# Kernel tuning notes

Measured on AMD Instinct MI355X. Metric: run time of the kernel, lower is better.

Reference implementation:

```python
import jax, jax.numpy as jnp
import numpy as np

H, I, B = 256, 128, 512

def setup_inputs() -> dict:
    key = jax.random.key(0)
    ks = jax.random.split(key, 24)
    n = lambda k, shp, s=1.0: jax.random.normal(k, shp, dtype=jnp.float32) * s
    inp = {
        "x": n(ks[0], (B, I)),
        "hx": n(ks[1], (B, H), 0.1),
        "cx": n(ks[2], (B, H, H), 0.1),
        # input->gate weights (hidden, input), xavier-like scale
        "Wii": n(ks[3], (H, I), (2.0 / (H + I)) ** 0.5),
        "Wif": n(ks[4], (H, I), (2.0 / (H + I)) ** 0.5),
        "Wig": n(ks[5], (H, I), (2.0 / (H + I)) ** 0.5),
        "Wio": n(ks[6], (H, I), (2.0 / (H + I)) ** 0.5),
        # hidden->gate weights (hidden, hidden), ~orthogonal scale
        "Whi": n(ks[7], (H, H), H ** -0.5),
        "Whit": n(ks[8], (H, H), H ** -0.5),
        "Whf": n(ks[9], (H, H), H ** -0.5),
        "Whft": n(ks[10], (H, H), H ** -0.5),
        "Whc": n(ks[11], (H, H), H ** -0.5),
        "Whct": n(ks[12], (H, H), H ** -0.5),
        "Who": n(ks[13], (H, H), H ** -0.5),
        "Uinv": n(ks[14], (H, H), H ** -0.5),
        "Vtinv": n(ks[15], (H, H), H ** -0.5),
        # biases: bi/bf/bg are full (H,H) matrices, bo is (H,1)
        "bi": jnp.zeros((H, H), jnp.float32),
        "bf": jnp.zeros((H, H), jnp.float32),
        "bg": jnp.zeros((H, H), jnp.float32),
        "bo": jnp.zeros((H, 1), jnp.float32),
    }
    return inp


def reference(x, hx, cx, Wii, Wif, Wig, Wio, Whi, Whit, Whf, Whft, Whc, Whct, Who, Uinv, Vtinv, bi, bf, bg, bo):
    # W @ diag(v) @ M^T  ==  einsum('hi,bi,gi->bhg', W, v, M)
    def sandwich(Wx, Wh, Wht, b):
        # (Wx*x) @ Wx^T + (Wh*hx) @ Wht^T + b  -> (B,H,H)
        xt = jnp.einsum('hi,bi,gi->bhg', Wx, x, Wx)
        ht = jnp.einsum('hj,bj,gj->bhg', Wh, hx, Wht)
        return xt + ht + b

    i = jax.nn.sigmoid(sandwich(Wii, Whi, Whit, bi))
    f = jax.nn.sigmoid(sandwich(Wif, Whf, Whft, bf))
    g = jnp.tanh(sandwich(Wig, Whc, Whct, bg))
    # o: ordinary vector gate (B,H)
    o = jax.nn.sigmoid(jnp.einsum('hi,bi->bh', Wio, x)
                       + jnp.einsum('hj,bj->bh', Who, hx) + bo[:, 0])
    cx_new = f * cx + i * g                     # (B,H,H)
    # diag(Uinv @ cx_new @ Vtinv) per batch element -> (B,H)
    proj_down = jnp.einsum('ij,bjk,ki->bi', Uinv, cx_new, Vtinv)
    hx_new = o * jax.nn.sigmoid(proj_down)
    return hx_new
```

## Files before the change

### kernel.cpp

```cpp
#include <hip/hip_runtime.h>
#include <hip/hip_bf16.h>

#define Hh 256
#define Ii 128
#define KF 384
#define KB 64
#define BK 64
#define LDSB 72

typedef __attribute__((ext_vector_type(8))) short bf16x8;
typedef __attribute__((ext_vector_type(4))) float f32x4;
typedef unsigned short u16;
typedef unsigned int u32;

__device__ inline float bf2f(u16 u) { return __uint_as_float(((u32)u) << 16); }
__device__ inline u16 f2bf(float f) {
  u32 u = __float_as_uint(f);
  u += 0x7FFFu + ((u >> 16) & 1u);
  return (u16)(u >> 16);
}
__device__ inline u32 pack_bf16x2(float a, float b) {
  __hip_bfloat162 h = __float22bfloat162_rn(make_float2(a, b));
  u32 r; __builtin_memcpy(&r, &h, 4); return r;
}
__device__ inline u32 scale2(u32 packed, float va, float vb) {
  float lo = __uint_as_float(packed << 16) * va;
  float hi = __uint_as_float(packed & 0xFFFF0000u) * vb;
  return pack_bf16x2(lo, hi);
}
__device__ inline float sigm(float x) { return 1.0f / (1.0f + __expf(-x)); }
__device__ inline float tanh_f(float x) { return 1.0f - 2.0f / (1.0f + __expf(2.0f * x)); }

union U32x4 { bf16x8 f; u32 d[4]; uint4 v; };

__global__ __launch_bounds__(256) void k_prep(
    const float* __restrict__ Wii, const float* __restrict__ Wif, const float* __restrict__ Wig,
    const float* __restrict__ Whi, const float* __restrict__ Whit,
    const float* __restrict__ Whf, const float* __restrict__ Whft,
    const float* __restrict__ Whc, const float* __restrict__ Whct,
    const float* __restrict__ Vtinv, const float* __restrict__ Uinv,
    const float* __restrict__ bi, const float* __restrict__ bfm, const float* __restrict__ bg,
    u16* __restrict__ RW, u16* __restrict__ CW, u16* __restrict__ Vtt,
    u16* __restrict__ biasP, float* __restrict__ UinvP, float* __restrict__ proj) {
  const int tid = threadIdx.x, bx = blockIdx.x, y = blockIdx.y;
  if (y < 3) {
    const float* WX  = (y == 0) ? Wii : (y == 1 ? Wif : Wig);
    const float* WHr = (y == 0) ? Whi : (y == 1 ? Whf : Whc);
    const float* WHt = (y == 0) ? Whit : (y == 1 ? Whft : Whct);
    u16* rw = RW + y * Hh * KF;
    u16* cw = CW + y * Hh * KF;
#pragma unroll
    for (int it = 0; it < 4; ++it) {
      int idx = it * 24576 + bx * 256 + tid;
      int h = idx / KF, t = idx - h * KF;
      float a, c;
      if (t < Ii) { a = WX[h * Ii + t]; c = a; }
      else        { a = WHr[h * Hh + t - Ii]; c = WHt[h * Hh + t - Ii]; }
      rw[idx] = f2bf(a);
      cw[idx] = f2bf(c);
    }
  } else if (y == 3) {
    if (bx < 64) {
      __shared__ u16 tbuf[32][33];
      const int c = tid & 31, r8 = tid >> 5;
      const int tr = bx >> 3, tc = bx & 7;
#pragma unroll
      for (int rr = r8; rr < 32; rr += 8)
        tbuf[rr][c] = f2bf(Vtinv[(tc * 32 + rr) * Hh + tr * 32 + c]);
      __syncthreads();
#pragma unroll
      for (int rr = r8; rr < 32; rr += 8)
        Vtt[(tr * 32 + rr) * Hh + tc * 32 + c] = tbuf[c][rr];
    } else if (bx < 96) {
      const int base = (bx - 64) * 256 + tid;
      const float4 z = {0.f, 0.f, 0.f, 0.f};
#pragma unroll
      for (int it = 0; it < 4; ++it)
        *(float4*)(proj + (size_t)(it * 8192 + base) * 4) = z;
    }
  } else if (y == 4) {
    const int base = (bx * 256 + tid) * 8;
#pragma unroll
    for (int e8 = 0; e8 < 8; ++e8) {
      int f = base + e8;
      int ph = f >> 16;
      int r1 = f & 65535;
      int jb = r1 >> 14;
      int r2 = r1 & 16383;
      int kb = r2 >> 12;
      int r3 = r2 & 4095;
      int t  = r3 >> 4;
      int e  = r3 & 15;
      int w = t >> 6, quad = (t >> 4) & 3, r15 = t & 15;
      int tk = e >> 2, rr = e & 3;
      int j   = jb * 64 + w * 16 + quad * 4 + rr;
      int col = kb * 64 + tk * 16 + r15;
      const float* src = (ph == 0) ? bg : (ph == 1 ? bi : bfm);
      biasP[f] = f2bf(src[j * Hh + col]);
    }
  } else {
    if (bx < 32) {
      const int base = (bx * 256 + tid) * 8;
#pragma unroll
      for (int e8 = 0; e8 < 8; ++e8) {
        int f = base + e8;
        int jb = f >> 14;
        int r2 = f & 16383;
        int t  = r2 >> 6;
        int e  = r2 & 63;
        int ti = e >> 4, tj = (e >> 2) & 3, rr = e & 3;
        int w = t >> 6, quad = (t >> 4) & 3, r15 = t & 15;
        int i = w * 64 + ti * 16 + quad * 4 + rr;
        int j = jb * 64 + tj * 16 + r15;
        UinvP[f] = Uinv[i * Hh + j];
      }
    }
  }
}

__global__ __launch_bounds__(256) void k_main(
    const float* __restrict__ x, const float* __restrict__ hx, const float* __restrict__ cx,
    const u16* __restrict__ RW, const u16* __restrict__ CW,
    const u16* __restrict__ Vtt, const u16* __restrict__ biasP,
    const float* __restrict__ UinvP, float* __restrict__ proj) {
  __shared__ u16 sB[2 * KB * LDSB];
  __shared__ u16 sP[KB * LDSB];
  __shared__ float sV[KF];

  const int tid  = threadIdx.x;
  const int b    = blockIdx.x >> 4;
  const int jb   = (blockIdx.x >> 2) & 3;
  const int kb   = blockIdx.x & 3;
  const int k0   = kb * KB;
  const int lane = tid & 63;
  const int w    = tid >> 6;
  const int r15  = lane & 15;
  const int quad = lane >> 4;
  const int jbase = jb * 64 + w * 16;
  const int brow = tid >> 2, bcg = tid & 3;

  if (tid < Ii) sV[tid] = x[b * Ii + tid];
  sV[Ii + tid] = hx[b * Hh + tid];

  const u16* rwp[3] = {RW + 2 * Hh * KF, RW, RW + 1 * Hh * KF};
  const u16* cwp[3] = {CW + 2 * Hh * KF, CW, CW + 1 * Hh * KF};
  const float* cx_b = cx + (size_t)b * Hh * Hh;

  __syncthreads();

  U32x4 n0, n1;
  {
    const u16* src = cwp[0] + (size_t)(k0 + brow) * KF + bcg * 16;
    n0.v = *(const uint4*)src;
    n1.v = *(const uint4*)(src + 8);
  }
  bf16x8 fa[2];
  fa[0] = *(const bf16x8*)(rwp[0] + (size_t)(jbase + r15) * KF + quad * 8);
  fa[1] = *(const bf16x8*)(rwp[0] + (size_t)(jbase + r15) * KF + 32 + quad * 8);
  {
    U32x4 o0, o1;
    const float4 v0 = *(const float4*)(&sV[bcg * 16]);
    const float4 v1 = *(const float4*)(&sV[bcg * 16 + 4]);
    const float4 v2 = *(const float4*)(&sV[bcg * 16 + 8]);
    const float4 v3 = *(const float4*)(&sV[bcg * 16 + 12]);
    o0.d[0] = scale2(n0.d[0], v0.x, v0.y); o0.d[1] = scale2(n0.d[1], v0.z, v0.w);
    o0.d[2] = scale2(n0.d[2], v1.x, v1.y); o0.d[3] = scale2(n0.d[3], v1.z, v1.w);
    o1.d[0] = scale2(n1.d[0], v2.x, v2.y); o1.d[1] = scale2(n1.d[1], v2.z, v2.w);
    o1.d[2] = scale2(n1.d[2], v3.x, v3.y); o1.d[3] = scale2(n1.d[3], v3.z, v3.w);
    u16* dst = sB + brow * LDSB + bcg * 16;
    *(uint4*)dst = o0.v;
    *(uint4*)(dst + 8) = o1.v;
  }
  __syncthreads();

  float p[4][4];

#pragma unroll
  for (int ph = 0; ph < 3; ++ph) {
    f32x4 acc[4];
#pragma unroll
    for (int tk = 0; tk < 4; ++tk)
#pragma unroll
      for (int r = 0; r < 4; ++r) acc[tk][r] = 0.0f;

#pragma unroll
    for (int kc = 0; kc < 6; ++kc) {
      const int sc = ph * 6 + kc;
      const int cur = sc & 1;
      const int nph = (kc < 5) ? ph : (ph < 2 ? ph + 1 : 0);
      const int nt0 = (kc < 5) ? (kc + 1) * BK : 0;
      U32x4 m0, m1;
      bf16x8 fan[2];
      if (sc < 17) {
        const u16* src = cwp[nph] + (size_t)(k0 + brow) * KF + nt0 + bcg * 16;
        m0.v = *(const uint4*)src;
        m1.v = *(const uint4*)(src + 8);
        fan[0] = *(const bf16x8*)(rwp[nph] + (size_t)(jbase + r15) * KF + nt0 + quad * 8);
        fan[1] = *(const bf16x8*)(rwp[nph] + (size_t)(jbase + r15) * KF + nt0 + 32 + quad * 8);
      }
#pragma unroll
      for (int ks = 0; ks < 2; ++ks) {
        bf16x8 fb[4];
#pragma unroll
        for (int tk = 0; tk < 4; ++tk)
          fb[tk] = *(const bf16x8*)(&sB[cur * (KB * LDSB) + (tk * 16 + r15) * LDSB + ks * 32 + quad * 8]);
#pragma unroll
        for (int tk = 0; tk < 4; ++tk)
          acc[tk] = __builtin_amdgcn_mfma_f32_16x16x32_bf16(fa[ks], fb[tk], acc[tk], 0, 0, 0);
      }
      if (sc < 17) {
        U32x4 o0, o1;
        const float4 v0 = *(const float4*)(&sV[nt0 + bcg * 16]);
        const float4 v1 = *(const float4*)(&sV[nt0 + bcg * 16 + 4]);
        const float4 v2 = *(const float4*)(&sV[nt0 + bcg * 16 + 8]);
        const float4 v3 = *(const float4*)(&sV[nt0 + bcg * 16 + 12]);
        o0.d[0] = scale2(m0.d[0], v0.x, v0.y); o0.d[1] = scale2(m0.d[1], v0.z, v0.w);
        o0.d[2] = scale2(m0.d[2], v1.x, v1.y); o0.d[3] = scale2(m0.d[3], v1.z, v1.w);
        o1.d[0] = scale2(m1.d[0], v2.x, v2.y); o1.d[1] = scale2(m1.d[1], v2.z, v2.w);
        o1.d[2] = scale2(m1.d[2], v3.x, v3.y); o1.d[3] = scale2(m1.d[3], v3.z, v3.w);
        u16* dst = sB + (cur ^ 1) * (KB * LDSB) + brow * LDSB + bcg * 16;
        *(uint4*)dst = o0.v;
        *(uint4*)(dst + 8) = o1.v;
        fa[0] = fan[0];
        fa[1] = fan[1];
      }
      if (kc == 5) {
        const u16* bp = biasP + ((size_t)((ph * 4 + jb) * 4 + kb) * 256 + tid) * 16;
        const uint4 b0 = *(const uint4*)bp;
        const uint4 b1 = *(const uint4*)(bp + 8);
        const u32 bw[8] = {b0.x, b0.y, b0.z, b0.w, b1.x, b1.y, b1.z, b1.w};
        if (ph == 2) {
          float cxv[16];
#pragma unroll
          for (int tk = 0; tk < 4; ++tk)
#pragma unroll
            for (int r = 0; r < 4; ++r)
              cxv[tk * 4 + r] = cx_b[(size_t)(jbase + quad * 4 + r) * Hh + k0 + tk * 16 + r15];
#pragma unroll
          for (int tk = 0; tk < 4; ++tk)
#pragma unroll
            for (int r = 0; r < 4; ++r) {
              const int e = tk * 4 + r;
              const float bias = (e & 1) ? __uint_as_float(bw[e >> 1] & 0xFFFF0000u)
                                         : __uint_as_float(bw[e >> 1] << 16);
              const float z = acc[tk][r] + bias;
              const float c = sigm(z) * cxv[e] + p[tk][r];
              sP[(w * 16 + quad * 4 + r) * LDSB + tk * 16 + r15] = f2bf(c);
            }
        } else {
#pragma unroll
          for (int tk = 0; tk < 4; ++tk)
#pragma unroll
            for (int r = 0; r < 4; ++r) {
              const int e = tk * 4 + r;
              const float bias = (e & 1) ? __uint_as_float(bw[e >> 1] & 0xFFFF0000u)
                                         : __uint_as_float(bw[e >> 1] << 16);
              const float z = acc[tk][r] + bias;
              if (ph == 0) p[tk][r] = tanh_f(z);
              else         p[tk][r] *= sigm(z);
            }
        }
      }
      __syncthreads();
    }
  }

  bf16x8 fbp[2][4];
#pragma unroll
  for (int ks = 0; ks < 2; ++ks)
#pragma unroll
    for (int tj = 0; tj < 4; ++tj)
      fbp[ks][tj] = *(const bf16x8*)(&sP[(tj * 16 + r15) * LDSB + ks * 32 + quad * 8]);

  float racc[4][4];
#pragma unroll
  for (int ti = 0; ti < 4; ++ti)
#pragma unroll
    for (int r = 0; r < 4; ++r) racc[ti][r] = 0.0f;

  const float* up = UinvP + ((size_t)jb * 256 + tid) * 64;
#pragma unroll
  for (int ti = 0; ti < 4; ++ti) {
    const bf16x8 va0 = *(const bf16x8*)(Vtt + (size_t)(w * 64 + ti * 16 + r15) * Hh + k0 + quad * 8);
    const bf16x8 va1 = *(const bf16x8*)(Vtt + (size_t)(w * 64 + ti * 16 + r15) * Hh + k0 + 32 + quad * 8);
    f32x4 pacc[4];
#pragma unroll
    for (int tj = 0; tj < 4; ++tj)
#pragma unroll
      for (int r = 0; r < 4; ++r) pacc[tj][r] = 0.0f;
#pragma unroll
    for (int tj = 0; tj < 4; ++tj)
      pacc[tj] = __builtin_amdgcn_mfma_f32_16x16x32_bf16(va0, fbp[0][tj], pacc[tj], 0, 0, 0);
#pragma unroll
    for (int tj = 0; tj < 4; ++tj)
      pacc[tj] = __builtin_amdgcn_mfma_f32_16x16x32_bf16(va1, fbp[1][tj], pacc[tj], 0, 0, 0);
    const float4 u0 = *(const float4*)(up + ti * 16);
    const float4 u1 = *(const float4*)(up + ti * 16 + 4);
    const float4 u2 = *(const float4*)(up + ti * 16 + 8);
    const float4 u3 = *(const float4*)(up + ti * 16 + 12);
    const float uu[16] = {u0.x, u0.y, u0.z, u0.w, u1.x, u1.y, u1.z, u1.w,
                          u2.x, u2.y, u2.z, u2.w, u3.x, u3.y, u3.z, u3.w};
#pragma unroll
    for (int tj = 0; tj < 4; ++tj)
#pragma unroll
      for (int r = 0; r < 4; ++r)
        racc[ti][r] += pacc[tj][r] * uu[tj * 4 + r];
  }

#pragma unroll
  for (int ti = 0; ti < 4; ++ti)
#pragma unroll
    for (int r = 0; r < 4; ++r) {
      float v = racc[ti][r];
      v += __shfl_xor(v, 1);
      v += __shfl_xor(v, 2);
      v += __shfl_xor(v, 4);
      v += __shfl_xor(v, 8);
      if (r15 == 0) atomicAdd(&proj[b * Hh + w * 64 + ti * 16 + quad * 4 + r], v);
    }
}

__global__ __launch_bounds__(256) void k_out(
    const float* __restrict__ x, const float* __restrict__ hx,
    const float* __restrict__ Wio, const float* __restrict__ Who,
    const float* __restrict__ bo, const float* __restrict__ proj,
    float* __restrict__ out) {
  __shared__ float sv[KF];
  const int b = blockIdx.x, tid = threadIdx.x;
  const int lane = tid & 63, w = tid >> 6;
  if (tid < Ii) sv[tid] = x[b * Ii + tid];
  sv[Ii + tid] = hx[b * Hh + tid];
  __syncthreads();
  for (int rr = 0; rr < 64; ++rr) {
    const int h = w * 64 + rr;
    float p = Wio[h * Ii + lane]        * sv[lane]
            + Wio[h * Ii + 64 + lane]   * sv[64 + lane]
            + Who[h * Hh + lane]        * sv[128 + lane]
            + Who[h * Hh + 64 + lane]   * sv[192 + lane]
            + Who[h * Hh + 128 + lane]  * sv[256 + lane]
            + Who[h * Hh + 192 + lane]  * sv[320 + lane];
    p += __shfl_xor(p, 32);
    p += __shfl_xor(p, 16);
    p += __shfl_xor(p, 8);
    p += __shfl_xor(p, 4);
    p += __shfl_xor(p, 2);
    p += __shfl_xor(p, 1);
    if (lane == 0)
      out[b * Hh + h] = sigm(p + bo[h]) * sigm(proj[b * Hh + h]);
  }
}

extern "C" void kernel_launch(void* const* d_in, const int* in_sizes, int n_in,
                              void* d_out, int out_size, void* d_ws, size_t ws_size,
                              hipStream_t stream) {
  (void)in_sizes; (void)n_in; (void)out_size; (void)ws_size;
  const float* x    = (const float*)d_in[0];
  const float* hx   = (const float*)d_in[1];
  const float* cx   = (const float*)d_in[2];
  const float* Wii  = (const float*)d_in[3];
  const float* Wif  = (const float*)d_in[4];
  const float* Wig  = (const float*)d_in[5];
  const float* Wio  = (const float*)d_in[6];
  const float* Whi  = (const float*)d_in[7];
  const float* Whit = (const float*)d_in[8];
  const float* Whf  = (const float*)d_in[9];
  const float* Whft = (const float*)d_in[10];
  const float* Whc  = (const float*)d_in[11];
  const float* Whct = (const float*)d_in[12];
  const float* Who  = (const float*)d_in[13];
  const float* Uinv = (const float*)d_in[14];
  const float* Vtinv= (const float*)d_in[15];
  const float* bi   = (const float*)d_in[16];
  const float* bf   = (const float*)d_in[17];
  const float* bg   = (const float*)d_in[18];
  const float* bo   = (const float*)d_in[19];
  float* out = (float*)d_out;

  u16* RW    = (u16*)d_ws;
  u16* CW    = RW + 3 * Hh * KF;
  u16* Vtt   = CW + 3 * Hh * KF;
  u16* biasP = Vtt + Hh * Hh;
  float* UinvP = (float*)(biasP + 3 * Hh * Hh);
  float* proj  = UinvP + Hh * Hh;

  k_prep<<<dim3(96, 6), 256, 0, stream>>>(Wii, Wif, Wig, Whi, Whit, Whf, Whft, Whc, Whct,
                                          Vtinv, Uinv, bi, bf, bg,
                                          RW, CW, Vtt, biasP, UinvP, proj);
  k_main<<<8192, 256, 0, stream>>>(x, hx, cx, RW, CW, Vtt, biasP, UinvP, proj);
  k_out<<<512, 256, 0, stream>>>(x, hx, Wio, Who, bo, proj, out);
}
```

Before: 563.0 us.

## Widen main kernel blocks to cover all 256 rows per batch-column tile

k_main now launches 2048 blocks of 512 threads, each covering the full 256-row j range for one batch and 64-column k slice, instead of 8192 blocks of 256 threads each covering 64 rows. The scaled cx-weight tile in LDS is built once per block and reused across four times as many rows, so the redundant global loads and rescaling are removed, and each wave now computes two 16-row MFMA tiles. Biases are read directly from the fp32 inputs rather than from a pre-permuted bf16 copy, so that prep step is dropped. Partial projection sums are combined in shared memory before a single atomic per output, which cuts atomic traffic. The cost is a larger sP buffer in LDS and more registers per thread, which may reduce occupancy.

```diff
diff --git a/kernel.cpp b/kernel.cpp
--- a/kernel.cpp
+++ b/kernel.cpp
@@ -4,8 +4,6 @@
 #define Hh 256
 #define Ii 128
 #define KF 384
-#define KB 64
-#define BK 64
 #define LDSB 72
 
 typedef __attribute__((ext_vector_type(8))) short bf16x8;
@@ -13,7 +11,6 @@
 typedef unsigned short u16;
 typedef unsigned int u32;
 
-__device__ inline float bf2f(u16 u) { return __uint_as_float(((u32)u) << 16); }
 __device__ inline u16 f2bf(float f) {
   u32 u = __float_as_uint(f);
   u += 0x7FFFu + ((u >> 16) & 1u);
@@ -39,9 +36,8 @@
     const float* __restrict__ Whf, const float* __restrict__ Whft,
     const float* __restrict__ Whc, const float* __restrict__ Whct,
     const float* __restrict__ Vtinv, const float* __restrict__ Uinv,
-    const float* __restrict__ bi, const float* __restrict__ bfm, const float* __restrict__ bg,
     u16* __restrict__ RW, u16* __restrict__ CW, u16* __restrict__ Vtt,
-    u16* __restrict__ biasP, float* __restrict__ UinvP, float* __restrict__ proj) {
+    float* __restrict__ UinvP, float* __restrict__ proj) {
   const int tid = threadIdx.x, bx = blockIdx.x, y = blockIdx.y;
   if (y < 3) {
     const float* WX  = (y == 0) ? Wii : (y == 1 ? Wif : Wig);
@@ -78,233 +74,197 @@
       for (int it = 0; it < 4; ++it)
         *(float4*)(proj + (size_t)(it * 8192 + base) * 4) = z;
     }
-  } else if (y == 4) {
-    const int base = (bx * 256 + tid) * 8;
-#pragma unroll
-    for (int e8 = 0; e8 < 8; ++e8) {
-      int f = base + e8;
-      int ph = f >> 16;
-      int r1 = f & 65535;
-      int jb = r1 >> 14;
-      int r2 = r1 & 16383;
-      int kb = r2 >> 12;
-      int r3 = r2 & 4095;
-      int t  = r3 >> 4;
-      int e  = r3 & 15;
-      int w = t >> 6, quad = (t >> 4) & 3, r15 = t & 15;
-      int tk = e >> 2, rr = e & 3;
-      int j   = jb * 64 + w * 16 + quad * 4 + rr;
-      int col = kb * 64 + tk * 16 + r15;
-      const float* src = (ph == 0) ? bg : (ph == 1 ? bi : bfm);
-      biasP[f] = f2bf(src[j * Hh + col]);
-    }
   } else {
     if (bx < 32) {
       const int base = (bx * 256 + tid) * 8;
 #pragma unroll
       for (int e8 = 0; e8 < 8; ++e8) {
         int f = base + e8;
-        int jb = f >> 14;
-        int r2 = f & 16383;
-        int t  = r2 >> 6;
-        int e  = r2 & 63;
-        int ti = e >> 4, tj = (e >> 2) & 3, rr = e & 3;
-        int w = t >> 6, quad = (t >> 4) & 3, r15 = t & 15;
-        int i = w * 64 + ti * 16 + quad * 4 + rr;
-        int j = jb * 64 + tj * 16 + r15;
+        int t512 = f >> 7;
+        int e = f & 127;
+        int ti = e >> 5;
+        int rem = e & 31;
+        int tjl = rem >> 2;
+        int rr = rem & 3;
+        int wv = t512 >> 6;
+        int ln = t512 & 63;
+        int qd = ln >> 4;
+        int r15v = ln & 15;
+        int i = (wv & 3) * 64 + ti * 16 + qd * 4 + rr;
+        int j = (wv >> 2) * 128 + tjl * 16 + r15v;
         UinvP[f] = Uinv[i * Hh + j];
       }
     }
   }
 }
 
-__global__ __launch_bounds__(256) void k_main(
+__global__ __launch_bounds__(512, 4) void k_main(
     const float* __restrict__ x, const float* __restrict__ hx, const float* __restrict__ cx,
-    const u16* __restrict__ RW, const u16* __restrict__ CW,
-    const u16* __restrict__ Vtt, const u16* __restrict__ biasP,
+    const u16* __restrict__ RW, const u16* __restrict__ CW, const u16* __restrict__ Vtt,
+    const float* __restrict__ bi, const float* __restrict__ bfm, const float* __restrict__ bg,
     const float* __restrict__ UinvP, float* __restrict__ proj) {
-  __shared__ u16 sB[2 * KB * LDSB];
-  __shared__ u16 sP[KB * LDSB];
+  __shared__ u16 sB[2 * 64 * LDSB];
+  __shared__ u16 sP[256 * LDSB];
   __shared__ float sV[KF];
+  __shared__ float sPart[8][64];
 
   const int tid  = threadIdx.x;
-  const int b    = blockIdx.x >> 4;
-  const int jb   = (blockIdx.x >> 2) & 3;
+  const int b    = blockIdx.x >> 2;
   const int kb   = blockIdx.x & 3;
-  const int k0   = kb * KB;
+  const int k0   = kb * 64;
   const int lane = tid & 63;
   const int w    = tid >> 6;
   const int r15  = lane & 15;
   const int quad = lane >> 4;
-  const int jbase = jb * 64 + w * 16;
-  const int brow = tid >> 2, bcg = tid & 3;
+  const int brow = tid >> 3, bcg = tid & 7;
 
   if (tid < Ii) sV[tid] = x[b * Ii + tid];
-  sV[Ii + tid] = hx[b * Hh + tid];
+  if (tid < Hh) sV[Ii + tid] = hx[b * Hh + tid];
 
   const u16* rwp[3] = {RW + 2 * Hh * KF, RW, RW + 1 * Hh * KF};
   const u16* cwp[3] = {CW + 2 * Hh * KF, CW, CW + 1 * Hh * KF};
+  const float* bp3[3] = {bg, bi, bfm};
   const float* cx_b = cx + (size_t)b * Hh * Hh;
 
+  U32x4 m;
+  m.v = *(const uint4*)(cwp[0] + (size_t)(k0 + brow) * KF + bcg * 8);
   __syncthreads();
-
-  U32x4 n0, n1;
   {
-    const u16* src = cwp[0] + (size_t)(k0 + brow) * KF + bcg * 16;
-    n0.v = *(const uint4*)src;
-    n1.v = *(const uint4*)(src + 8);
-  }
-  bf16x8 fa[2];
-  fa[0] = *(const bf16x8*)(rwp[0] + (size_t)(jbase + r15) * KF + quad * 8);
-  fa[1] = *(const bf16x8*)(rwp[0] + (size_t)(jbase + r15) * KF + 32 + quad * 8);
-  {
-    U32x4 o0, o1;
-    const float4 v0 = *(const float4*)(&sV[bcg * 16]);
-    const float4 v1 = *(const float4*)(&sV[bcg * 16 + 4]);
-    const float4 v2 = *(const float4*)(&sV[bcg * 16 + 8]);
-    const float4 v3 = *(const float4*)(&sV[bcg * 16 + 12]);
-    o0.d[0] = scale2(n0.d[0], v0.x, v0.y); o0.d[1] = scale2(n0.d[1], v0.z, v0.w);
-    o0.d[2] = scale2(n0.d[2], v1.x, v1.y); o0.d[3] = scale2(n0.d[3], v1.z, v1.w);
-    o1.d[0] = scale2(n1.d[0], v2.x, v2.y); o1.d[1] = scale2(n1.d[1], v2.z, v2.w);
-    o1.d[2] = scale2(n1.d[2], v3.x, v3.y); o1.d[3] = scale2(n1.d[3], v3.z, v3.w);
-    u16* dst = sB + brow * LDSB + bcg * 16;
-    *(uint4*)dst = o0.v;
-    *(uint4*)(dst + 8) = o1.v;
+    U32x4 o;
+    const float4 va = *(const float4*)(&sV[bcg * 8]);
+    const float4 vb = *(const float4*)(&sV[bcg * 8 + 4]);
+    o.d[0] = scale2(m.d[0], va.x, va.y); o.d[1] = scale2(m.d[1], va.z, va.w);
+    o.d[2] = scale2(m.d[2], vb.x, vb.y); o.d[3] = scale2(m.d[3], vb.z, vb.w);
+    *(uint4*)(&sB[brow * LDSB + bcg * 8]) = o.v;
   }
   __syncthreads();
 
-  float p[4][4];
+  float p[2][4][4];
+  const size_t wrow = (size_t)(w * 32 + r15) * KF;
 
 #pragma unroll
   for (int ph = 0; ph < 3; ++ph) {
-    f32x4 acc[4];
-#pragma unroll
-    for (int tk = 0; tk < 4; ++tk)
-#pragma unroll
-      for (int r = 0; r < 4; ++r) acc[tk][r] = 0.0f;
+    f32x4 acc[2][4];
+#pragma unroll
+    for (int ja = 0; ja < 2; ++ja)
+#pragma unroll
+      for (int tk = 0; tk < 4; ++tk)
+#pragma unroll
+        for (int r = 0; r < 4; ++r) acc[ja][tk][r] = 0.0f;
 
 #pragma unroll
     for (int kc = 0; kc < 6; ++kc) {
-      const int sc = ph * 6 + kc;
+      const int sc  = ph * 6 + kc;
       const int cur = sc & 1;
+      const int t0  = kc * 64;
       const int nph = (kc < 5) ? ph : (ph < 2 ? ph + 1 : 0);
-      const int nt0 = (kc < 5) ? (kc + 1) * BK : 0;
-      U32x4 m0, m1;
-      bf16x8 fan[2];
+      const int nt0 = (kc < 5) ? t0 + 64 : 0;
+      U32x4 mn;
+      if (sc < 17)
+        mn.v = *(const uint4*)(cwp[nph] + (size_t)(k0 + brow) * KF + nt0 + bcg * 8);
+      bf16x8 wf[2][2];
+#pragma unroll
+      for (int ja = 0; ja < 2; ++ja)
+#pragma unroll
+        for (int ks = 0; ks < 2; ++ks)
+          wf[ja][ks] = *(const bf16x8*)(rwp[ph] + wrow + (size_t)ja * 16 * KF + t0 + ks * 32 + quad * 8);
+#pragma unroll
+      for (int ks = 0; ks < 2; ++ks) {
+        bf16x8 sf[4];
+#pragma unroll
+        for (int tk = 0; tk < 4; ++tk)
+          sf[tk] = *(const bf16x8*)(&sB[cur * (64 * LDSB) + (tk * 16 + r15) * LDSB + ks * 32 + quad * 8]);
+#pragma unroll
+        for (int tk = 0; tk < 4; ++tk) {
+          acc[0][tk] = __builtin_amdgcn_mfma_f32_16x16x32_bf16(sf[tk], wf[0][ks], acc[0][tk], 0, 0, 0);
+          acc[1][tk] = __builtin_amdgcn_mfma_f32_16x16x32_bf16(sf[tk], wf[1][ks], acc[1][tk], 0, 0, 0);
+        }
+      }
       if (sc < 17) {
-        const u16* src = cwp[nph] + (size_t)(k0 + brow) * KF + nt0 + bcg * 16;
-        m0.v = *(const uint4*)src;
-        m1.v = *(const uint4*)(src + 8);
-        fan[0] = *(const bf16x8*)(rwp[nph] + (size_t)(jbase + r15) * KF + nt0 + quad * 8);
-        fan[1] = *(const bf16x8*)(rwp[nph] + (size_t)(jbase + r15) * KF + nt0 + 32 + quad * 8);
-      }
-#pragma unroll
-      for (int ks = 0; ks < 2; ++ks) {
-        bf16x8 fb[4];
-#pragma unroll
-        for (int tk = 0; tk < 4; ++tk)
-          fb[tk] = *(const bf16x8*)(&sB[cur * (KB * LDSB) + (tk * 16 + r15) * LDSB + ks * 32 + quad * 8]);
-#pragma unroll
-        for (int tk = 0; tk < 4; ++tk)
-          acc[tk] = __builtin_amdgcn_mfma_f32_16x16x32_bf16(fa[ks], fb[tk], acc[tk], 0, 0, 0);
-      }
-      if (sc < 17) {
-        U32x4 o0, o1;
-        const float4 v0 = *(const float4*)(&sV[nt0 + bcg * 16]);
-        const float4 v1 = *(const float4*)(&sV[nt0 + bcg * 16 + 4]);
-        const float4 v2 = *(const float4*)(&sV[nt0 + bcg * 16 + 8]);
-        const float4 v3 = *(const float4*)(&sV[nt0 + bcg * 16 + 12]);
-        o0.d[0] = scale2(m0.d[0], v0.x, v0.y); o0.d[1] = scale2(m0.d[1], v0.z, v0.w);
-        o0.d[2] = scale2(m0.d[2], v1.x, v1.y); o0.d[3] = scale2(m0.d[3], v1.z, v1.w);
-        o1.d[0] = scale2(m1.d[0], v2.x, v2.y); o1.d[1] = scale2(m1.d[1], v2.z, v2.w);
-        o1.d[2] = scale2(m1.d[2], v3.x, v3.y); o1.d[3] = scale2(m1.d[3], v3.z, v3.w);
-        u16* dst = sB + (cur ^ 1) * (KB * LDSB) + brow * LDSB + bcg * 16;
-        *(uint4*)dst = o0.v;
-        *(uint4*)(dst + 8) = o1.v;
-        fa[0] = fan[0];
-        fa[1] = fan[1];
+        U32x4 o;
+        const float4 va = *(const float4*)(&sV[nt0 + bcg * 8]);
+        const float4 vb = *(const float4*)(&sV[nt0 + bcg * 8 + 4]);
+        o.d[0] = scale2(mn.d[0], va.x, va.y); o.d[1] = scale2(mn.d[1], va.z, va.w);
+        o.d[2] = scale2(mn.d[2], vb.x, vb.y); o.d[3] = scale2(mn.d[3], vb.z, vb.w);
+        *(uint4*)(&sB[(cur ^ 1) * (64 * LDSB) + brow * LDSB + bcg * 8]) = o.v;
       }
       if (kc == 5) {
-        const u16* bp = biasP + ((size_t)((ph * 4 + jb) * 4 + kb) * 256 + tid) * 16;
-        const uint4 b0 = *(const uint4*)bp;
-        const uint4 b1 = *(const uint4*)(bp + 8);
-        const u32 bw[8] = {b0.x, b0.y, b0.z, b0.w, b1.x, b1.y, b1.z, b1.w};
-        if (ph == 2) {
-          float cxv[16];
-#pragma unroll
-          for (int tk = 0; tk < 4; ++tk)
-#pragma unroll
-            for (int r = 0; r < 4; ++r)
-              cxv[tk * 4 + r] = cx_b[(size_t)(jbase + quad * 4 + r) * Hh + k0 + tk * 16 + r15];
-#pragma unroll
-          for (int tk = 0; tk < 4; ++tk)
-#pragma unroll
-            for (int r = 0; r < 4; ++r) {
-              const int e = tk * 4 + r;
-              const float bias = (e & 1) ? __uint_as_float(bw[e >> 1] & 0xFFFF0000u)
-                                         : __uint_as_float(bw[e >> 1] << 16);
-              const float z = acc[tk][r] + bias;
-              const float c = sigm(z) * cxv[e] + p[tk][r];
-              sP[(w * 16 + quad * 4 + r) * LDSB + tk * 16 + r15] = f2bf(c);
+        const float* bp = bp3[ph];
+#pragma unroll
+        for (int ja = 0; ja < 2; ++ja) {
+          const int jg = w * 32 + ja * 16 + r15;
+          const float* bpr = bp + (size_t)jg * Hh + k0 + quad * 4;
+          const float* cxr = cx_b + (size_t)jg * Hh + k0 + quad * 4;
+#pragma unroll
+          for (int tk = 0; tk < 4; ++tk) {
+            const float4 bv = *(const float4*)(bpr + tk * 16);
+            if (ph == 0) {
+#pragma unroll
+              for (int r = 0; r < 4; ++r)
+                p[ja][tk][r] = tanh_f(acc[ja][tk][r] + ((const float*)&bv)[r]);
+            } else if (ph == 1) {
+#pragma unroll
+              for (int r = 0; r < 4; ++r)
+                p[ja][tk][r] *= sigm(acc[ja][tk][r] + ((const float*)&bv)[r]);
+            } else {
+              const float4 cv = *(const float4*)(cxr + tk * 16);
+              float cc[4];
+#pragma unroll
+              for (int r = 0; r < 4; ++r)
+                cc[r] = sigm(acc[ja][tk][r] + ((const float*)&bv)[r]) * ((const float*)&cv)[r] + p[ja][tk][r];
+              uint2 pk;
+              pk.x = pack_bf16x2(cc[0], cc[1]);
+              pk.y = pack_bf16x2(cc[2], cc[3]);
+              *(uint2*)(&sP[jg * LDSB + tk * 16 + quad * 4]) = pk;
             }
-        } else {
-#pragma unroll
-          for (int tk = 0; tk < 4; ++tk)
-#pragma unroll
-            for (int r = 0; r < 4; ++r) {
-              const int e = tk * 4 + r;
-              const float bias = (e & 1) ? __uint_as_float(bw[e >> 1] & 0xFFFF0000u)
-                                         : __uint_as_float(bw[e >> 1] << 16);
-              const float z = acc[tk][r] + bias;
-              if (ph == 0) p[tk][r] = tanh_f(z);
-              else         p[tk][r] *= sigm(z);
-            }
+          }
         }
       }
       __syncthreads();
     }
   }
 
-  bf16x8 fbp[2][4];
-#pragma unroll
-  for (int ks = 0; ks < 2; ++ks)
-#pragma unroll
-    for (int tj = 0; tj < 4; ++tj)
-      fbp[ks][tj] = *(const bf16x8*)(&sP[(tj * 16 + r15) * LDSB + ks * 32 + quad * 8]);
-
+  const int islab = (w & 3) * 64;
+  const int jhb   = (w >> 2) * 128;
+  const float* up = UinvP + (size_t)tid * 128;
   float racc[4][4];
 #pragma unroll
   for (int ti = 0; ti < 4; ++ti)
 #pragma unroll
     for (int r = 0; r < 4; ++r) racc[ti][r] = 0.0f;
 
-  const float* up = UinvP + ((size_t)jb * 256 + tid) * 64;
-#pragma unroll
-  for (int ti = 0; ti < 4; ++ti) {
-    const bf16x8 va0 = *(const bf16x8*)(Vtt + (size_t)(w * 64 + ti * 16 + r15) * Hh + k0 + quad * 8);
-    const bf16x8 va1 = *(const bf16x8*)(Vtt + (size_t)(w * 64 + ti * 16 + r15) * Hh + k0 + 32 + quad * 8);
-    f32x4 pacc[4];
-#pragma unroll
-    for (int tj = 0; tj < 4; ++tj)
-#pragma unroll
-      for (int r = 0; r < 4; ++r) pacc[tj][r] = 0.0f;
-#pragma unroll
-    for (int tj = 0; tj < 4; ++tj)
-      pacc[tj] = __builtin_amdgcn_mfma_f32_16x16x32_bf16(va0, fbp[0][tj], pacc[tj], 0, 0, 0);
-#pragma unroll
-    for (int tj = 0; tj < 4; ++tj)
-      pacc[tj] = __builtin_amdgcn_mfma_f32_16x16x32_bf16(va1, fbp[1][tj], pacc[tj], 0, 0, 0);
-    const float4 u0 = *(const float4*)(up + ti * 16);
-    const float4 u1 = *(const float4*)(up + ti * 16 + 4);
-    const float4 u2 = *(const float4*)(up + ti * 16 + 8);
-    const float4 u3 = *(const float4*)(up + ti * 16 + 12);
-    const float uu[16] = {u0.x, u0.y, u0.z, u0.w, u1.x, u1.y, u1.z, u1.w,
-                          u2.x, u2.y, u2.z, u2.w, u3.x, u3.y, u3.z, u3.w};
-#pragma unroll
-    for (int tj = 0; tj < 4; ++tj)
-#pragma unroll
-      for (int r = 0; r < 4; ++r)
-        racc[ti][r] += pacc[tj][r] * uu[tj * 4 + r];
+#pragma unroll
+  for (int tjg = 0; tjg < 2; ++tjg) {
+    bf16x8 fbp[2][4];
+#pragma unroll
+    for (int ks = 0; ks < 2; ++ks)
+#pragma unroll
+      for (int tjj = 0; tjj < 4; ++tjj)
+        fbp[ks][tjj] = *(const bf16x8*)(&sP[(jhb + (tjg * 4 + tjj) * 16 + r15) * LDSB + ks * 32 + quad * 8]);
+#pragma unroll
+    for (int ti = 0; ti < 4; ++ti) {
+      const u16* vrow = Vtt + (size_t)(islab + ti * 16 + r15) * Hh + k0 + quad * 8;
+      const bf16x8 va0 = *(const bf16x8*)vrow;
+      const bf16x8 va1 = *(const bf16x8*)(vrow + 32);
+      f32x4 pacc[4];
+#pragma unroll
+      for (int tjj = 0; tjj < 4; ++tjj)
+#pragma unroll
+        for (int r = 0; r < 4; ++r) pacc[tjj][r] = 0.0f;
+#pragma unroll
+      for (int tjj = 0; tjj < 4; ++tjj)
+        pacc[tjj] = __builtin_amdgcn_mfma_f32_16x16x32_bf16(va0, fbp[0][tjj], pacc[tjj], 0, 0, 0);
+#pragma unroll
+      for (int tjj = 0; tjj < 4; ++tjj)
+        pacc[tjj] = __builtin_amdgcn_mfma_f32_16x16x32_bf16(va1, fbp[1][tjj], pacc[tjj], 0, 0, 0);
+#pragma unroll
+      for (int tjj = 0; tjj < 4; ++tjj) {
+        const float4 uu = *(const float4*)(up + ti * 32 + (tjg * 4 + tjj) * 4);
+#pragma unroll
+        for (int r = 0; r < 4; ++r)
+          racc[ti][r] += pacc[tjj][r] * ((const float*)&uu)[r];
+      }
+    }
   }
 
 #pragma unroll
@@ -316,8 +276,11 @@
       v += __shfl_xor(v, 2);
       v += __shfl_xor(v, 4);
       v += __shfl_xor(v, 8);
-      if (r15 == 0) atomicAdd(&proj[b * Hh + w * 64 + ti * 16 + quad * 4 + r], v);
-    }
+      if (r15 == 0) sPart[w][ti * 16 + quad * 4 + r] = v;
+    }
+  __syncthreads();
+  if (tid < Hh)
+    atomicAdd(&proj[b * Hh + tid], sPart[tid >> 6][tid & 63] + sPart[(tid >> 6) + 4][tid & 63]);
 }
 
 __global__ __launch_bounds__(256) void k_out(
@@ -379,13 +342,11 @@
   u16* RW    = (u16*)d_ws;
   u16* CW    = RW + 3 * Hh * KF;
   u16* Vtt   = CW + 3 * Hh * KF;
-  u16* biasP = Vtt + Hh * Hh;
-  float* UinvP = (float*)(biasP + 3 * Hh * Hh);
+  float* UinvP = (float*)(Vtt + Hh * Hh);
   float* proj  = UinvP + Hh * Hh;
 
-  k_prep<<<dim3(96, 6), 256, 0, stream>>>(Wii, Wif, Wig, Whi, Whit, Whf, Whft, Whc, Whct,
-                                          Vtinv, Uinv, bi, bf, bg,
-                                          RW, CW, Vtt, biasP, UinvP, proj);
-  k_main<<<8192, 256, 0, stream>>>(x, hx, cx, RW, CW, Vtt, biasP, UinvP, proj);
+  k_prep<<<dim3(96, 5), 256, 0, stream>>>(Wii, Wif, Wig, Whi, Whit, Whf, Whft, Whc, Whct,
+                                          Vtinv, Uinv, RW, CW, Vtt, UinvP, proj);
+  k_main<<<2048, 512, 0, stream>>>(x, hx, cx, RW, CW, Vtt, bi, bf, bg, UinvP, proj);
   k_out<<<512, 256, 0, stream>>>(x, hx, Wio, Who, bo, proj, out);
 }
```

After: 983.9 us. +74.8%, slower.
